# Kernel tuning notes

Measured on AMD Instinct MI355X. Metric: run time of the kernel, lower is better.

Reference implementation:

```python
import jax, jax.numpy as jnp
import numpy as np

# Dimensions (see shape_source): B=4, fine grid 8x8 windows of 16x16 tokens,
# pooled by 4x4 -> global grid 32x32 -> 2x2 windows of 16x16 tokens.
B, H, W, M, C, NH = 4, 8, 8, 16, 256, 8
HD = C // NH
GW = 2  # global window grid (2x2)


def _ln(x, g, b):
    m = x.mean(-1, keepdims=True)
    v = ((x - m) ** 2).mean(-1, keepdims=True)
    return (x - m) / jnp.sqrt(v + 1e-5) * g + b


def _posemb(x, w1, b1, w2):
    # RelativePositionEmbed: MLP(2 -> 512 -> C) over normalized 2D coords.
    N = x.shape[1]
    ctx = int(round(N ** 0.5))
    half = ctx // 2
    r = jnp.arange(ctx, dtype=x.dtype)
    grid = jnp.stack(jnp.meshgrid(r, r, indexing='ij'))  # [2, ctx, ctx]
    coords = ((grid - half) / half).reshape(2, -1).T     # [N, 2]
    return x + jax.nn.relu(coords @ w1 + b1) @ w2


def _mlp(x, w1, b1, w2, b2):
    return jax.nn.gelu(x @ w1 + b1, approximate=False) @ w2 + b2


def _sattn_block(x, ln1g, ln1b, wqkv, bqkv, wo, bo, ln2g, ln2b, mw1, mb1, mw2, mb2):
    # Pre-norm windowed MHSA + MLP (all2all self-attention inside each window).
    bn, N, _ = x.shape
    h = _ln(x, ln1g, ln1b)
    q, k, v = jnp.split(h @ wqkv + bqkv, 3, axis=-1)
    q = q.reshape(bn, N, NH, HD)
    k = k.reshape(bn, N, NH, HD)
    v = v.reshape(bn, N, NH, HD)
    att = jax.nn.softmax(jnp.einsum('bnhd,bmhd->bhnm', q, k) / (HD ** 0.5), axis=-1)
    o = jnp.einsum('bhnm,bmhd->bnhd', att, v).reshape(bn, N, C)
    x = x + o @ wo + bo
    return x + _mlp(_ln(x, ln2g, ln2b), mw1, mb1, mw2, mb2)


def _forward(scale0, scale1, pe_w1, pe_b1, pe_w2, ln1_g, ln1_b, wqkv, bqkv,
             wo, bo, ln2_g, ln2_b, mlp_w1, mlp_b1, mlp_w2, mlp_b2):
    # 1) per-scale relative position embeddings (weight_share=False path)
    x0 = _posemb(scale0, pe_w1[0], pe_b1[0], pe_w2[0])  # [B*64, 256, C]
    x1 = _posemb(scale1, pe_w1[1], pe_b1[1], pe_w2[1])  # [B*4, 256, C]

    # 2) propagate_bottom_up: max-pool each 16x16 window by 4 -> 4x4,
    p = x0.reshape(B * H * W, 4, 4, 4, 4, C).max(axis=(2, 4))  # (r1,p1,r2,p2)->max over p
    p = p.reshape(B, H, W, 4, 4, C).transpose(0, 1, 3, 2, 4, 5).reshape(B, H * 4, W * 4, C)
    l2g = p.reshape(B, GW, M, GW, M, C).transpose(0, 1, 3, 2, 4, 5).reshape(B * GW * GW, M * M, C)
    x1 = x1 + l2g

    # 3) all2all self-attention per scale (coarse to fine order; independent)
    o1 = _sattn_block(x1, ln1_g[1], ln1_b[1], wqkv[1], bqkv[1], wo[1], bo[1],
                      ln2_g[1], ln2_b[1], mlp_w1[1], mlp_b1[1], mlp_w2[1], mlp_b2[1])
    o0 = _sattn_block(x0, ln1_g[0], ln1_b[0], wqkv[0], bqkv[0], wo[0], bo[0],
                      ln2_g[0], ln2_b[0], mlp_w1[0], mlp_b1[0], mlp_w2[0], mlp_b2[0])

    # 4) one2one cross-attention aggregation: each global token queries the
    #    4x4 fine-token region it was pooled from (one-to-one mapping).
    fine = o0.reshape(B, H, W, 4, 4, 4, 4, C).transpose(0, 1, 2, 3, 5, 4, 6, 7)
    fine = fine.reshape(B * H * W * 16, 16, C)  # [B*1024, 16, C], order (b,h,w,r1,r2)
    g = o1.reshape(B, GW, GW, M, M, C).transpose(0, 1, 3, 2, 4, 5).reshape(B, 32, 32, C)
    g = g.reshape(B, H, 4, W, 4, C).transpose(0, 1, 3, 2, 4, 5).reshape(B * H * W * 16, 1, C)

    qn = _ln(g, ln1_g[1], ln1_b[1])
    kn = _ln(fine, ln1_g[1], ln1_b[1])
    wq, wk, wv = jnp.split(wqkv[1], 3, axis=-1)
    bq, bk, bv = jnp.split(bqkv[1], 3)
    q = (qn @ wq + bq).reshape(-1, 1, NH, HD)
    k = (kn @ wk + bk).reshape(-1, 16, NH, HD)
    v = (kn @ wv + bv).reshape(-1, 16, NH, HD)
    att = jax.nn.softmax(jnp.einsum('bnhd,bmhd->bhnm', q, k) / (HD ** 0.5), axis=-1)
    o = jnp.einsum('bhnm,bmhd->bnhd', att, v).reshape(-1, 1, C)
    g = g + o @ wo[1] + bo[1]
    g = g + _mlp(_ln(g, ln2_g[1], ln2_b[1]), mlp_w1[1], mlp_b1[1], mlp_w2[1], mlp_b2[1])

    # back to global window layout [B*4, 256, C]
    g = g.reshape(B, H, W, 4, 4, C).transpose(0, 1, 3, 2, 4, 5).reshape(B, 32, 32, C)
    o1 = g.reshape(B, GW, M, GW, M, C).transpose(0, 1, 3, 2, 4, 5).reshape(B * GW * GW, M * M, C)

    # concat on window axis so the harness sees a single output array
    return jnp.concatenate([o0, o1], axis=0)  # [272, 256, C]


def setup_inputs() -> dict:
    key = jax.random.key(0)
    ks = jax.random.split(key, 8)

    def w(k, shape):
        return jax.random.normal(k, shape, jnp.float32) * 0.02

    return {
        'scale0': jax.random.normal(ks[0], (B * H * W, M * M, C), jnp.float32),
        'scale1': jax.random.normal(ks[1], (B * GW * GW, M * M, C), jnp.float32),
        'pe_w1': w(ks[2], (2, 2, 512)), 'pe_b1': jnp.zeros((2, 512), jnp.float32),
        'pe_w2': w(ks[3], (2, 512, C)),
        'ln1_g': jnp.ones((2, C), jnp.float32), 'ln1_b': jnp.zeros((2, C), jnp.float32),
        'wqkv': w(ks[4], (2, C, 3 * C)), 'bqkv': jnp.zeros((2, 3 * C), jnp.float32),
        'wo': w(ks[5], (2, C, C)), 'bo': jnp.zeros((2, C), jnp.float32),
        'ln2_g': jnp.ones((2, C), jnp.float32), 'ln2_b': jnp.zeros((2, C), jnp.float32),
        'mlp_w1': w(ks[6], (2, C, 4 * C)), 'mlp_b1': jnp.zeros((2, 4 * C), jnp.float32),
        'mlp_w2': w(ks[7], (2, 4 * C, C)), 'mlp_b2': jnp.zeros((2, C), jnp.float32),
    }


def reference(scale0, scale1, pe_w1, pe_b1, pe_w2, ln1_g, ln1_b, wqkv, bqkv,
              wo, bo, ln2_g, ln2_b, mlp_w1, mlp_b1, mlp_w2, mlp_b2):
    return _forward(scale0, scale1, pe_w1, pe_b1, pe_w2, ln1_g, ln1_b, wqkv,
                    bqkv, wo, bo, ln2_g, ln2_b, mlp_w1, mlp_b1, mlp_w2, mlp_b2)
```

## Files before the change

### kernel.cpp

```cpp
#include <hip/hip_runtime.h>
#include <hip/hip_bf16.h>
#include <hip/hip_fp16.h>

#define ROWS0 65536
#define ROWS1 4096

typedef _Float16 half8 __attribute__((ext_vector_type(8)));
typedef _Float16 half4_t __attribute__((ext_vector_type(4)));
typedef float floatx4 __attribute__((ext_vector_type(4)));

#define LDSP(p) ((__attribute__((address_space(3))) void*)(p))
#define GLBP(p) ((const __attribute__((address_space(1))) void*)(p))

__device__ __forceinline__ float gelu_f(float x) {
    float t = x * (1.595769122f + 0.071354816f * x * x);
    return x / (1.0f + __expf(-t));
}

__global__ __launch_bounds__(256) void pe_kernel(
    const float* __restrict__ w1, const float* __restrict__ b1,
    const float* __restrict__ w2, float* __restrict__ pe)
{
    __shared__ float hid[512];
    int blk = blockIdx.x;
    int s = blk >> 8, n = blk & 255;
    int i = n >> 4, j = n & 15;
    float c0 = (i - 8) * 0.125f;
    float c1 = (j - 8) * 0.125f;
    int t = threadIdx.x;
    for (int hh = t; hh < 512; hh += 256) {
        float hv = c0 * w1[s * 1024 + hh] + c1 * w1[s * 1024 + 512 + hh] + b1[s * 512 + hh];
        hid[hh] = fmaxf(hv, 0.f);
    }
    __syncthreads();
    float o = 0.f;
    const float* w2p = w2 + (size_t)s * 512 * 256 + t;
    #pragma unroll 8
    for (int hh = 0; hh < 512; hh++) o += hid[hh] * w2p[hh * 256];
    pe[(size_t)s * 65536 + n * 256 + t] = o;
}

__global__ __launch_bounds__(256) void add_pe0_kernel(
    const float* __restrict__ s0, const float* __restrict__ pe, float* __restrict__ out)
{
    int row = blockIdx.x, c = threadIdx.x;
    out[(size_t)row * 256 + c] = s0[(size_t)row * 256 + c] + pe[(row & 255) * 256 + c];
}

__global__ __launch_bounds__(256) void pool_kernel(
    const float* __restrict__ x0, const float* __restrict__ s1,
    const float* __restrict__ pe1, float* __restrict__ x1out)
{
    int w1 = blockIdx.x >> 8, n1 = blockIdx.x & 255, c = threadIdx.x;
    int b = w1 >> 2, wy = (w1 >> 1) & 1, wx = w1 & 1;
    int ty = n1 >> 4, tx = n1 & 15;
    int gy = wy * 16 + ty, gx = wx * 16 + tx;
    int h = gy >> 2, r1 = gy & 3, w = gx >> 2, r2 = gx & 3;
    int fw = (b * 8 + h) * 8 + w;
    const float* base = x0 + ((size_t)fw * 256 + r1 * 64 + r2 * 4) * 256 + c;
    float mv = -1e30f;
    #pragma unroll
    for (int p1 = 0; p1 < 4; p1++)
        #pragma unroll
        for (int p2 = 0; p2 < 4; p2++)
            mv = fmaxf(mv, base[(p1 * 16 + p2) * 256]);
    size_t oidx = ((size_t)w1 * 256 + n1) * 256 + c;
    x1out[oidx] = s1[oidx] + pe1[n1 * 256 + c] + mv;
}

__global__ __launch_bounds__(256) void ln16_kernel(
    const float* __restrict__ X, const float* __restrict__ g,
    const float* __restrict__ b, _Float16* __restrict__ Y)
{
    __shared__ float smr[4];
    int row = blockIdx.x, t = threadIdx.x;
    float x = X[(size_t)row * 256 + t];
    float v = x;
    for (int o = 32; o; o >>= 1) v += __shfl_down(v, o);
    if ((t & 63) == 0) smr[t >> 6] = v;
    __syncthreads();
    float mean = (smr[0] + smr[1] + smr[2] + smr[3]) * (1.0f / 256.0f);
    __syncthreads();
    float d = x - mean;
    float vv = d * d;
    for (int o = 32; o; o >>= 1) vv += __shfl_down(vv, o);
    if ((t & 63) == 0) smr[t >> 6] = vv;
    __syncthreads();
    float var = (smr[0] + smr[1] + smr[2] + smr[3]) * (1.0f / 256.0f);
    float inv = 1.0f / sqrtf(var + 1e-5f);
    Y[(size_t)row * 256 + t] = (_Float16)(d * inv * g[t] + b[t]);
}

__global__ __launch_bounds__(256) void transposeW_kernel(
    const float* __restrict__ src, _Float16* __restrict__ dst, int K, int N)
{
    __shared__ float t[32][33];
    int k0 = blockIdx.y * 32, n0 = blockIdx.x * 32;
    int tx = threadIdx.x & 31, ty = threadIdx.x >> 5;
    for (int r = ty; r < 32; r += 8) t[r][tx] = src[(size_t)(k0 + r) * N + n0 + tx];
    __syncthreads();
    for (int r = ty; r < 32; r += 8) dst[(size_t)(n0 + r) * K + k0 + tx] = (_Float16)t[tx][r];
}

template<int ACT, int RES, int OUT16>
__global__ __launch_bounds__(256) void hgemm_kernel(
    const _Float16* __restrict__ A, const _Float16* __restrict__ Bw,
    const float* __restrict__ bias, const float* __restrict__ Res,
    void* __restrict__ Yv, int M, int N, int K)
{
    __shared__ alignas(16) _Float16 smem[4 * 4096];
    int tid = threadIdx.x;

    int gx = N >> 7;
    int nwg = gx * (M >> 7);
    int q8 = nwg >> 3;
    int wg = (blockIdx.x & 7) * q8 + (blockIdx.x >> 3);
    int m0 = (wg / gx) << 7, n0 = (wg % gx) << 7;

    int wave = tid >> 6, lane = tid & 63;
    int wr = wave >> 1, wc = wave & 1;
    int r = lane & 15, c = lane >> 4;
    floatx4 acc[4][4] = {};

    const int NT = K >> 5;

    auto stage = [&](int buf, int t) {
        int k0 = t << 5;
        #pragma unroll
        for (int p = 0; p < 2; p++) {
            int s = tid + (p << 8);
            int row = s >> 2, phys = s & 3;
            int logc = phys ^ (row & 3);
            const _Float16* ga = A + (size_t)(m0 + row) * K + k0 + logc * 8;
            __builtin_amdgcn_global_load_lds(GLBP(ga), LDSP(&smem[buf * 4096 + s * 8]), 16, 0, 0);
            const _Float16* gb = Bw + (size_t)(n0 + row) * K + k0 + logc * 8;
            __builtin_amdgcn_global_load_lds(GLBP(gb), LDSP(&smem[8192 + buf * 4096 + s * 8]), 16, 0, 0);
        }
    };

    stage(0, 0);
    __syncthreads();
    int cur = 0;
    for (int t = 0; t < NT; t++) {
        if (t + 1 < NT) stage(cur ^ 1, t + 1);
        const _Float16* As = &smem[cur * 4096];
        const _Float16* Bs = &smem[8192 + cur * 4096];
        half8 af[4], bf[4];
        #pragma unroll
        for (int i = 0; i < 4; i++) {
            int ra = wr * 64 + i * 16 + r;
            af[i] = *(const half8*)&As[ra * 32 + ((c ^ (ra & 3)) << 3)];
            int rb = wc * 64 + i * 16 + r;
            bf[i] = *(const half8*)&Bs[rb * 32 + ((c ^ (rb & 3)) << 3)];
        }
        #pragma unroll
        for (int i = 0; i < 4; i++)
            #pragma unroll
            for (int j = 0; j < 4; j++)
                acc[i][j] = __builtin_amdgcn_mfma_f32_16x16x32_f16(af[i], bf[j], acc[i][j], 0, 0, 0);
        __syncthreads();
        cur ^= 1;
    }

    int qrow = lane >> 4;
    if (OUT16) {
        _Float16* sth = smem + wave * 1152;
        #pragma unroll
        for (int i = 0; i < 4; i++) {
            #pragma unroll
            for (int j = 0; j < 4; j++) {
                float bj = bias[n0 + wc * 64 + j * 16 + r];
                #pragma unroll
                for (int reg = 0; reg < 4; reg++) {
                    float v = acc[i][j][reg] + bj;
                    if (ACT) v = gelu_f(v);
                    sth[(qrow * 4 + reg) * 72 + j * 16 + r] = (_Float16)v;
                }
            }
            #pragma unroll
            for (int p = 0; p < 2; p++) {
                int row = p * 8 + (lane >> 3);
                half8 hv = *(const half8*)&sth[row * 72 + (lane & 7) * 8];
                *(half8*)((_Float16*)Yv + (size_t)(m0 + wr * 64 + i * 16 + row) * N
                          + n0 + wc * 64 + (lane & 7) * 8) = hv;
            }
        }
    } else {
        float* stf = (float*)smem + wave * 1088;
        #pragma unroll
        for (int i = 0; i < 4; i++) {
            #pragma unroll
            for (int j = 0; j < 4; j++) {
                float bj = bias[n0 + wc * 64 + j * 16 + r];
                #pragma unroll
                for (int reg = 0; reg < 4; reg++) {
                    float v = acc[i][j][reg] + bj;
                    if (ACT) v = gelu_f(v);
                    stf[(qrow * 4 + reg) * 68 + j * 16 + r] = v;
                }
            }
            #pragma unroll
            for (int p = 0; p < 4; p++) {
                int row = p * 4 + (lane >> 4);
                float4 fv = *(const float4*)&stf[row * 68 + (lane & 15) * 4];
                size_t ga = (size_t)(m0 + wr * 64 + i * 16 + row) * N
                            + n0 + wc * 64 + (lane & 15) * 4;
                if (RES) {
                    float4 rv = *(const float4*)(Res + ga);
                    fv.x += rv.x; fv.y += rv.y; fv.z += rv.z; fv.w += rv.w;
                }
                *(float4*)((float*)Yv + ga) = fv;
            }
        }
    }
}

__global__ __launch_bounds__(256) void attn_mfma_kernel(
    const _Float16* __restrict__ qkv, _Float16* __restrict__ out)
{
    __shared__ alignas(16) _Float16 Klds[8192];
    __shared__ alignas(16) _Float16 Qlds[8192];
    __shared__ alignas(16) _Float16 VT[8192];
    __shared__ alignas(16) _Float16 Pl[4][4096];

    int tid = threadIdx.x;
    int win = blockIdx.x, head = blockIdx.y;
    int w = tid >> 6, lane = tid & 63;
    int r = lane & 15, h = lane >> 4;

    {
        const _Float16* base = qkv + ((size_t)(win * 256 + tid)) * 768 + head * 32;
        half8 qv[4], kv[4], vv[4];
        #pragma unroll
        for (int c = 0; c < 4; c++) {
            qv[c] = *(const half8*)(base + c * 8);
            kv[c] = *(const half8*)(base + 256 + c * 8);
            vv[c] = *(const half8*)(base + 512 + c * 8);
        }
        int rowbase = (tid >> 1) * 64;
        #pragma unroll
        for (int c = 0; c < 4; c++) {
            int phys = (((tid & 1) << 2) + c) ^ ((tid >> 1) & 7);
            *(half8*)&Qlds[rowbase + phys * 8] = qv[c];
            *(half8*)&Klds[rowbase + phys * 8] = kv[c];
        }
        #pragma unroll
        for (int d = 0; d < 32; d++)
            VT[d * 256 + (((tid >> 3) ^ (d & 7)) << 3) + (tid & 7)] = vv[d >> 3][d & 7];
    }
    __syncthreads();

    half8 vf[2][8];
    #pragma unroll
    for (int dc = 0; dc < 2; dc++)
        #pragma unroll
        for (int kc2 = 0; kc2 < 8; kc2++)
            vf[dc][kc2] = *(const half8*)&VT[(dc * 16 + r) * 256 + ((((kc2 << 2) + h) ^ (r & 7)) << 3)];

    const floatx4 zf = {0.f, 0.f, 0.f, 0.f};
    int physa = (((r & 1) << 2) + h) ^ ((r >> 1) & 7);

    for (int g = 0; g < 4; g++) {
        int qg = (w << 2) + g;
        half8 qb = *(const half8*)&Qlds[((qg << 3) + (r >> 1)) * 64 + physa * 8];
        floatx4 s[16];
        #pragma unroll
        for (int kc = 0; kc < 16; kc++) {
            half8 ka = *(const half8*)&Klds[((kc << 3) + (r >> 1)) * 64 + physa * 8];
            s[kc] = __builtin_amdgcn_mfma_f32_16x16x32_f16(ka, qb, zf, 0, 0, 0);
        }
        float m = -1e30f;
        #pragma unroll
        for (int kc = 0; kc < 16; kc++)
            #pragma unroll
            for (int e = 0; e < 4; e++) m = fmaxf(m, s[kc][e]);
        m = fmaxf(m, __shfl_xor(m, 16));
        m = fmaxf(m, __shfl_xor(m, 32));
        float l = 0.f;
        #pragma unroll
        for (int kc = 0; kc < 16; kc++)
            #pragma unroll
            for (int e = 0; e < 4; e++) {
                float p = __expf((s[kc][e] - m) * 0.17677669529663687f);
                s[kc][e] = p;
                l += p;
            }
        l += __shfl_xor(l, 16);
        l += __shfl_xor(l, 32);
        float inv = 1.0f / l;
        #pragma unroll
        for (int kc = 0; kc < 16; kc++) {
            half4_t pk;
            pk[0] = (_Float16)s[kc][0]; pk[1] = (_Float16)s[kc][1];
            pk[2] = (_Float16)s[kc][2]; pk[3] = (_Float16)s[kc][3];
            *(half4_t*)&Pl[w][r * 256 + ((((kc << 1) + (h >> 1)) ^ (r & 7)) << 3) + ((h & 1) << 2)] = pk;
        }
        floatx4 o0 = zf, o1 = zf;
        #pragma unroll
        for (int kc2 = 0; kc2 < 8; kc2++) {
            half8 pb = *(const half8*)&Pl[w][r * 256 + ((((kc2 << 2) + h) ^ (r & 7)) << 3)];
            o0 = __builtin_amdgcn_mfma_f32_16x16x32_f16(vf[0][kc2], pb, o0, 0, 0, 0);
            o1 = __builtin_amdgcn_mfma_f32_16x16x32_f16(vf[1][kc2], pb, o1, 0, 0, 0);
        }
        #pragma unroll
        for (int dc = 0; dc < 2; dc++) {
            floatx4 o = dc ? o1 : o0;
            half4_t oh;
            #pragma unroll
            for (int e = 0; e < 4; e++) oh[e] = (_Float16)(o[e] * inv);
            *(half4_t*)&Pl[w][(r >> 1) * 64 + (((((r & 1) << 2) + (dc << 1) + (h >> 1)) ^ ((r >> 1) & 7)) << 3) + ((h & 1) << 2)] = oh;
        }
        int q2 = lane >> 2, c2 = lane & 3;
        half8 ov = *(const half8*)&Pl[w][(q2 >> 1) * 64 + (((((q2 & 1) << 2) + c2) ^ ((q2 >> 1) & 7)) << 3)];
        *(half8*)(out + ((size_t)(win * 256 + qg * 16 + q2)) * 256 + head * 32 + c2 * 8) = ov;
    }
}

__global__ __launch_bounds__(128) void cross_attn_kernel(
    const _Float16* __restrict__ Qb, const _Float16* __restrict__ KV,
    _Float16* __restrict__ Ob, int fw0)
{
    __shared__ float att_s[8][16];
    int t = threadIdx.x;
    int lw = blockIdx.x >> 4;
    int sub = blockIdx.x & 15;
    int r1 = sub >> 2, r2 = sub & 3;
    int gi = (fw0 + lw) * 16 + sub;
    int h = t >> 4, m = t & 15;
    int p1 = m >> 2, p2 = m & 3;
    int lr = lw * 256 + r1 * 64 + p1 * 16 + r2 * 4 + p2;
    const half8* qp = (const half8*)(Qb + (size_t)gi * 256 + h * 32);
    const half8* kp = (const half8*)(KV + (size_t)lr * 512 + h * 32);
    float sc = 0.f;
    #pragma unroll
    for (int d8 = 0; d8 < 4; d8++) {
        half8 qv = qp[d8], kv = kp[d8];
        #pragma unroll
        for (int j = 0; j < 8; j++) sc += (float)qv[j] * (float)kv[j];
    }
    sc *= 0.17677669529663687f;
    float mx = sc;
    for (int o = 8; o; o >>= 1) mx = fmaxf(mx, __shfl_xor(mx, o));
    float e = __expf(sc - mx);
    float ssum = e;
    for (int o = 8; o; o >>= 1) ssum += __shfl_xor(ssum, o);
    att_s[h][m] = e / ssum;
    __syncthreads();
    int dg = t & 15;
    int d0 = dg * 2;
    float o0 = 0.f, o1 = 0.f;
    #pragma unroll
    for (int mm = 0; mm < 16; mm++) {
        int pp1 = mm >> 2, pp2 = mm & 3;
        int lrr = lw * 256 + r1 * 64 + pp1 * 16 + r2 * 4 + pp2;
        const _Float16* vp = KV + (size_t)lrr * 512 + 256 + h * 32;
        float a = att_s[h][mm];
        o0 += a * (float)vp[d0];
        o1 += a * (float)vp[d0 + 1];
    }
    Ob[(size_t)gi * 256 + h * 32 + d0]     = (_Float16)o0;
    Ob[(size_t)gi * 256 + h * 32 + d0 + 1] = (_Float16)o1;
}

__global__ __launch_bounds__(256) void gather_g_kernel(
    const float* __restrict__ o1, float* __restrict__ G)
{
    int gi = blockIdx.x, c = threadIdx.x;
    int b = gi >> 10, rem = gi & 1023;
    int h = rem >> 7, w = (rem >> 4) & 7, r1 = (rem >> 2) & 3, r2 = rem & 3;
    int gy = h * 4 + r1, gx = w * 4 + r2;
    int w1 = (b * 2 + (gy >> 4)) * 2 + (gx >> 4);
    int n1 = (gy & 15) * 16 + (gx & 15);
    G[(size_t)gi * 256 + c] = o1[((size_t)w1 * 256 + n1) * 256 + c];
}

__global__ __launch_bounds__(256) void scatter_g_kernel(
    const float* __restrict__ G, float* __restrict__ o1)
{
    int gi = blockIdx.x, c = threadIdx.x;
    int b = gi >> 10, rem = gi & 1023;
    int h = rem >> 7, w = (rem >> 4) & 7, r1 = (rem >> 2) & 3, r2 = rem & 3;
    int gy = h * 4 + r1, gx = w * 4 + r2;
    int w1 = (b * 2 + (gy >> 4)) * 2 + (gx >> 4);
    int n1 = (gy & 15) * 16 + (gx & 15);
    o1[((size_t)w1 * 256 + n1) * 256 + c] = G[(size_t)gi * 256 + c];
}

extern "C" void kernel_launch(void* const* d_in, const int* in_sizes, int n_in,
                              void* d_out, int out_size, void* d_ws, size_t ws_size,
                              hipStream_t stream)
{
    const float* scale0 = (const float*)d_in[0];
    const float* scale1 = (const float*)d_in[1];
    const float* pe_w1  = (const float*)d_in[2];
    const float* pe_b1  = (const float*)d_in[3];
    const float* pe_w2  = (const float*)d_in[4];
    const float* ln1_g  = (const float*)d_in[5];
    const float* ln1_b  = (const float*)d_in[6];
    const float* wqkv   = (const float*)d_in[7];
    const float* bqkv   = (const float*)d_in[8];
    const float* wo     = (const float*)d_in[9];
    const float* bo     = (const float*)d_in[10];
    const float* ln2_g  = (const float*)d_in[11];
    const float* ln2_b  = (const float*)d_in[12];
    const float* mw1    = (const float*)d_in[13];
    const float* mb1    = (const float*)d_in[14];
    const float* mw2    = (const float*)d_in[15];
    const float* mb2    = (const float*)d_in[16];
    float* out = (float*)d_out;
    char* arena = (char*)d_ws;

    float*    PE     = (float*)arena;              arena += 131072 * 4;
    float*    G      = (float*)arena;              arena += (size_t)4096 * 256 * 4;
    _Float16* Q16    = (_Float16*)arena;           arena += (size_t)4096 * 256 * 2;
    _Float16* OX16   = (_Float16*)arena;           arena += (size_t)4096 * 256 * 2;
    _Float16* wqkvT  = (_Float16*)arena;           arena += (size_t)2 * 768 * 256 * 2;
    _Float16* woT    = (_Float16*)arena;           arena += (size_t)2 * 256 * 256 * 2;
    _Float16* mw1T   = (_Float16*)arena;           arena += (size_t)2 * 1024 * 256 * 2;
    _Float16* mw2T   = (_Float16*)arena;           arena += (size_t)2 * 256 * 1024 * 2;
    size_t fixed_bytes = (size_t)(arena - (char*)d_ws);

    int R = 8192;
    if (fixed_bytes + (size_t)65536 * 4608 <= ws_size) R = 65536;
    else if (fixed_bytes + (size_t)32768 * 4608 <= ws_size) R = 32768;
    else if (fixed_bytes + (size_t)16384 * 4608 <= ws_size) R = 16384;
    int NC = 65536 / R;
    int CW = R / 256;

    _Float16* bufH16 = (_Float16*)arena;           arena += (size_t)R * 256 * 2;
    _Float16* qkv16  = (_Float16*)arena;           arena += (size_t)R * 768 * 2;
    _Float16* hid16  = (_Float16*)arena;           arena += (size_t)R * 1024 * 2;
    _Float16* o16    = (_Float16*)arena;

    auto hgemm = [&](const _Float16* A, const _Float16* Bw, const float* bias,
                     const float* Res, void* Y, int M, int N, int K, int act) {
        int nwg = (N >> 7) * (M >> 7);
        if (act)           hgemm_kernel<1, 0, 1><<<nwg, 256, 0, stream>>>(A, Bw, bias, nullptr, Y, M, N, K);
        else if (Res)      hgemm_kernel<0, 1, 0><<<nwg, 256, 0, stream>>>(A, Bw, bias, Res, Y, M, N, K);
        else               hgemm_kernel<0, 0, 1><<<nwg, 256, 0, stream>>>(A, Bw, bias, nullptr, Y, M, N, K);
    };

    auto sattn = [&](float* x, int Mrows, int nw, int s) {
        ln16_kernel<<<Mrows, 256, 0, stream>>>(x, ln1_g + s * 256, ln1_b + s * 256, bufH16);
        hgemm(bufH16, wqkvT + (size_t)s * 196608, bqkv + s * 768, nullptr, qkv16, Mrows, 768, 256, 0);
        attn_mfma_kernel<<<dim3(nw, 8), 256, 0, stream>>>(qkv16, o16);
        hgemm(o16, woT + (size_t)s * 65536, bo + s * 256, x, x, Mrows, 256, 256, 0);
        ln16_kernel<<<Mrows, 256, 0, stream>>>(x, ln2_g + s * 256, ln2_b + s * 256, bufH16);
        hgemm(bufH16, mw1T + (size_t)s * 262144, mb1 + s * 1024, nullptr, hid16, Mrows, 1024, 256, 1);
        hgemm(hid16, mw2T + (size_t)s * 262144, mb2 + s * 256, x, x, Mrows, 256, 1024, 0);
    };

    float* o1sec = out + (size_t)ROWS0 * 256;

    transposeW_kernel<<<dim3(768 / 32, 256 / 32), 256, 0, stream>>>(wqkv, wqkvT, 256, 768);
    transposeW_kernel<<<dim3(768 / 32, 256 / 32), 256, 0, stream>>>(wqkv + 196608, wqkvT + 196608, 256, 768);
    transposeW_kernel<<<dim3(256 / 32, 256 / 32), 256, 0, stream>>>(wo, woT, 256, 256);
    transposeW_kernel<<<dim3(256 / 32, 256 / 32), 256, 0, stream>>>(wo + 65536, woT + 65536, 256, 256);
    transposeW_kernel<<<dim3(1024 / 32, 256 / 32), 256, 0, stream>>>(mw1, mw1T, 256, 1024);
    transposeW_kernel<<<dim3(1024 / 32, 256 / 32), 256, 0, stream>>>(mw1 + 262144, mw1T + 262144, 256, 1024);
    transposeW_kernel<<<dim3(256 / 32, 1024 / 32), 256, 0, stream>>>(mw2, mw2T, 1024, 256);
    transposeW_kernel<<<dim3(256 / 32, 1024 / 32), 256, 0, stream>>>(mw2 + 262144, mw2T + 262144, 1024, 256);

    pe_kernel<<<512, 256, 0, stream>>>(pe_w1, pe_b1, pe_w2, PE);
    add_pe0_kernel<<<ROWS0, 256, 0, stream>>>(scale0, PE, out);
    pool_kernel<<<ROWS1, 256, 0, stream>>>(out, scale1, PE + 65536, o1sec);

    sattn(o1sec, ROWS1, 16, 1);
    for (int c = 0; c < NC; c++)
        sattn(out + (size_t)c * R * 256, R, CW, 0);

    gather_g_kernel<<<4096, 256, 0, stream>>>(o1sec, G);
    ln16_kernel<<<4096, 256, 0, stream>>>(G, ln1_g + 256, ln1_b + 256, bufH16);
    hgemm(bufH16, wqkvT + 196608, bqkv + 768, nullptr, Q16, 4096, 256, 256, 0);
    for (int c = 0; c < NC; c++) {
        float* xch = out + (size_t)c * R * 256;
        ln16_kernel<<<R, 256, 0, stream>>>(xch, ln1_g + 256, ln1_b + 256, bufH16);
        hgemm(bufH16, wqkvT + 196608 + 65536, bqkv + 768 + 256, nullptr, qkv16, R, 512, 256, 0);
        cross_attn_kernel<<<CW * 16, 128, 0, stream>>>(Q16, qkv16, OX16, c * CW);
    }
    hgemm(OX16, woT + 65536, bo + 256, G, G, 4096, 256, 256, 0);
    ln16_kernel<<<4096, 256, 0, stream>>>(G, ln2_g + 256, ln2_b + 256, bufH16);
    hgemm(bufH16, mw1T + 262144, mb1 + 1024, nullptr, hid16, 4096, 1024, 256, 1);
    hgemm(hid16, mw2T + 262144, mb2 + 256, G, G, 4096, 256, 1024, 0);
    scatter_g_kernel<<<4096, 256, 0, stream>>>(G, o1sec);
}
```

Baseline: 865.1 us.

## Use head-major QKV/output layout, split attention queries across two blocks, tree-reduce softmax

The QKV GEMM now writes its output in a head-major planar layout ([head][token][32]), and the attention kernel writes its output in that layout too. The output-projection GEMM reads its A operand in the same planar form, and cross-attention reads K/V from planes. Self-attention blocks now each handle half of a window's queries, which doubles the grid and halves Q shared memory. The P buffer is padded to reduce LDS bank conflicts, and the softmax max/sum reductions use a tree form with a fused scale. The aim is contiguous per-head loads, more parallelism and fewer LDS conflicts, at the cost of each block reloading K/V for its window.

```diff
diff --git a/kernel.cpp b/kernel.cpp
--- a/kernel.cpp
+++ b/kernel.cpp
@@ -16,6 +16,13 @@
     float t = x * (1.595769122f + 0.071354816f * x * x);
     return x / (1.0f + __expf(-t));
 }
+__device__ __forceinline__ floatx4 max4(floatx4 a, floatx4 b) {
+    floatx4 r;
+    r[0] = fmaxf(a[0], b[0]); r[1] = fmaxf(a[1], b[1]);
+    r[2] = fmaxf(a[2], b[2]); r[3] = fmaxf(a[3], b[3]);
+    return r;
+}
+__device__ __forceinline__ floatx4 add4(floatx4 a, floatx4 b) { return a + b; }
 
 __global__ __launch_bounds__(256) void pe_kernel(
     const float* __restrict__ w1, const float* __restrict__ b1,
@@ -102,11 +109,11 @@
     for (int r = ty; r < 32; r += 8) dst[(size_t)(n0 + r) * K + k0 + tx] = (_Float16)t[tx][r];
 }
 
-template<int ACT, int RES, int OUT16>
+template<int ACT, int RES, int OUT16, int ALAY, int OLAY>
 __global__ __launch_bounds__(256) void hgemm_kernel(
     const _Float16* __restrict__ A, const _Float16* __restrict__ Bw,
     const float* __restrict__ bias, const float* __restrict__ Res,
-    void* __restrict__ Yv, int M, int N, int K)
+    void* __restrict__ Yv, int M, int N, int K, size_t aps, size_t ops)
 {
     __shared__ alignas(16) _Float16 smem[4 * 4096];
     int tid = threadIdx.x;
@@ -131,7 +138,9 @@
             int s = tid + (p << 8);
             int row = s >> 2, phys = s & 3;
             int logc = phys ^ (row & 3);
-            const _Float16* ga = A + (size_t)(m0 + row) * K + k0 + logc * 8;
+            const _Float16* ga;
+            if (ALAY) ga = A + (size_t)(k0 >> 5) * aps + ((size_t)(m0 + row) << 5) + logc * 8;
+            else      ga = A + (size_t)(m0 + row) * K + k0 + logc * 8;
             __builtin_amdgcn_global_load_lds(GLBP(ga), LDSP(&smem[buf * 4096 + s * 8]), 16, 0, 0);
             const _Float16* gb = Bw + (size_t)(n0 + row) * K + k0 + logc * 8;
             __builtin_amdgcn_global_load_lds(GLBP(gb), LDSP(&smem[8192 + buf * 4096 + s * 8]), 16, 0, 0);
@@ -181,8 +190,12 @@
             for (int p = 0; p < 2; p++) {
                 int row = p * 8 + (lane >> 3);
                 half8 hv = *(const half8*)&sth[row * 72 + (lane & 7) * 8];
-                *(half8*)((_Float16*)Yv + (size_t)(m0 + wr * 64 + i * 16 + row) * N
-                          + n0 + wc * 64 + (lane & 7) * 8) = hv;
+                int grow = m0 + wr * 64 + i * 16 + row;
+                int col8 = n0 + wc * 64 + (lane & 7) * 8;
+                _Float16* dst;
+                if (OLAY) dst = (_Float16*)Yv + (size_t)(col8 >> 5) * ops + ((size_t)grow << 5) + (col8 & 31);
+                else      dst = (_Float16*)Yv + (size_t)grow * N + col8;
+                *(half8*)dst = hv;
             }
         }
     } else {
@@ -216,37 +229,40 @@
 }
 
 __global__ __launch_bounds__(256) void attn_mfma_kernel(
-    const _Float16* __restrict__ qkv, _Float16* __restrict__ out)
+    const _Float16* __restrict__ qkv, _Float16* __restrict__ out, const size_t ps)
 {
     __shared__ alignas(16) _Float16 Klds[8192];
-    __shared__ alignas(16) _Float16 Qlds[8192];
+    __shared__ alignas(16) _Float16 Qlds[4096];
     __shared__ alignas(16) _Float16 VT[8192];
-    __shared__ alignas(16) _Float16 Pl[4][4096];
+    __shared__ alignas(16) _Float16 Pl[4][4224];
 
     int tid = threadIdx.x;
-    int win = blockIdx.x, head = blockIdx.y;
+    int win = blockIdx.x >> 1, qhalf = blockIdx.x & 1, head = blockIdx.y;
     int w = tid >> 6, lane = tid & 63;
     int r = lane & 15, h = lane >> 4;
 
     {
-        const _Float16* base = qkv + ((size_t)(win * 256 + tid)) * 768 + head * 32;
-        half8 qv[4], kv[4], vv[4];
-        #pragma unroll
-        for (int c = 0; c < 4; c++) {
-            qv[c] = *(const half8*)(base + c * 8);
-            kv[c] = *(const half8*)(base + 256 + c * 8);
-            vv[c] = *(const half8*)(base + 512 + c * 8);
-        }
+        const half8* kp8 = (const half8*)(qkv + (size_t)(8 + head) * ps + (((size_t)win * 256 + tid) << 5));
+        const half8* vp8 = (const half8*)(qkv + (size_t)(16 + head) * ps + (((size_t)win * 256 + tid) << 5));
+        half8 kv[4], vv[4];
+        #pragma unroll
+        for (int c = 0; c < 4; c++) { kv[c] = kp8[c]; vv[c] = vp8[c]; }
         int rowbase = (tid >> 1) * 64;
         #pragma unroll
         for (int c = 0; c < 4; c++) {
             int phys = (((tid & 1) << 2) + c) ^ ((tid >> 1) & 7);
-            *(half8*)&Qlds[rowbase + phys * 8] = qv[c];
             *(half8*)&Klds[rowbase + phys * 8] = kv[c];
         }
         #pragma unroll
         for (int d = 0; d < 32; d++)
             VT[d * 256 + (((tid >> 3) ^ (d & 7)) << 3) + (tid & 7)] = vv[d >> 3][d & 7];
+        int local = tid >> 1;
+        const half8* qp8 = (const half8*)(qkv + (size_t)head * ps
+                            + (((size_t)win * 256 + qhalf * 128 + local) << 5) + (tid & 1) * 16);
+        half8 q0 = qp8[0], q1 = qp8[1];
+        int rb = (local >> 1) * 64, c0 = (tid & 1) * 2;
+        *(half8*)&Qlds[rb + (((((local & 1) << 2) + c0)) ^ ((local >> 1) & 7)) * 8] = q0;
+        *(half8*)&Qlds[rb + (((((local & 1) << 2) + c0 + 1)) ^ ((local >> 1) & 7)) * 8] = q1;
     }
     __syncthreads();
 
@@ -258,10 +274,11 @@
             vf[dc][kc2] = *(const half8*)&VT[(dc * 16 + r) * 256 + ((((kc2 << 2) + h) ^ (r & 7)) << 3)];
 
     const floatx4 zf = {0.f, 0.f, 0.f, 0.f};
+    const float SCALE = 0.17677669529663687f;
     int physa = (((r & 1) << 2) + h) ^ ((r >> 1) & 7);
 
-    for (int g = 0; g < 4; g++) {
-        int qg = (w << 2) + g;
+    for (int g = 0; g < 2; g++) {
+        int qg = (w << 1) + g;
         half8 qb = *(const half8*)&Qlds[((qg << 3) + (r >> 1)) * 64 + physa * 8];
         floatx4 s[16];
         #pragma unroll
@@ -269,22 +286,27 @@
             half8 ka = *(const half8*)&Klds[((kc << 3) + (r >> 1)) * 64 + physa * 8];
             s[kc] = __builtin_amdgcn_mfma_f32_16x16x32_f16(ka, qb, zf, 0, 0, 0);
         }
-        float m = -1e30f;
-        #pragma unroll
-        for (int kc = 0; kc < 16; kc++)
-            #pragma unroll
-            for (int e = 0; e < 4; e++) m = fmaxf(m, s[kc][e]);
+        floatx4 t8[8];
+        #pragma unroll
+        for (int i = 0; i < 8; i++) t8[i] = max4(s[2 * i], s[2 * i + 1]);
+        #pragma unroll
+        for (int i = 0; i < 4; i++) t8[i] = max4(t8[i], t8[i + 4]);
+        t8[0] = max4(max4(t8[0], t8[2]), max4(t8[1], t8[3]));
+        float m = fmaxf(fmaxf(t8[0][0], t8[0][1]), fmaxf(t8[0][2], t8[0][3]));
         m = fmaxf(m, __shfl_xor(m, 16));
         m = fmaxf(m, __shfl_xor(m, 32));
-        float l = 0.f;
+        float msc = m * SCALE;
         #pragma unroll
         for (int kc = 0; kc < 16; kc++)
             #pragma unroll
-            for (int e = 0; e < 4; e++) {
-                float p = __expf((s[kc][e] - m) * 0.17677669529663687f);
-                s[kc][e] = p;
-                l += p;
-            }
+            for (int e = 0; e < 4; e++)
+                s[kc][e] = __expf(fmaf(s[kc][e], SCALE, -msc));
+        #pragma unroll
+        for (int i = 0; i < 8; i++) t8[i] = add4(s[2 * i], s[2 * i + 1]);
+        #pragma unroll
+        for (int i = 0; i < 4; i++) t8[i] = add4(t8[i], t8[i + 4]);
+        t8[0] = add4(add4(t8[0], t8[2]), add4(t8[1], t8[3]));
+        float l = (t8[0][0] + t8[0][1]) + (t8[0][2] + t8[0][3]);
         l += __shfl_xor(l, 16);
         l += __shfl_xor(l, 32);
         float inv = 1.0f / l;
@@ -293,12 +315,12 @@
             half4_t pk;
             pk[0] = (_Float16)s[kc][0]; pk[1] = (_Float16)s[kc][1];
             pk[2] = (_Float16)s[kc][2]; pk[3] = (_Float16)s[kc][3];
-            *(half4_t*)&Pl[w][r * 256 + ((((kc << 1) + (h >> 1)) ^ (r & 7)) << 3) + ((h & 1) << 2)] = pk;
+            *(half4_t*)&Pl[w][r * 264 + ((((kc << 1) + (h >> 1)) ^ (r & 7)) << 3) + ((h & 1) << 2)] = pk;
         }
         floatx4 o0 = zf, o1 = zf;
         #pragma unroll
         for (int kc2 = 0; kc2 < 8; kc2++) {
-            half8 pb = *(const half8*)&Pl[w][r * 256 + ((((kc2 << 2) + h) ^ (r & 7)) << 3)];
+            half8 pb = *(const half8*)&Pl[w][r * 264 + ((((kc2 << 2) + h) ^ (r & 7)) << 3)];
             o0 = __builtin_amdgcn_mfma_f32_16x16x32_f16(vf[0][kc2], pb, o0, 0, 0, 0);
             o1 = __builtin_amdgcn_mfma_f32_16x16x32_f16(vf[1][kc2], pb, o1, 0, 0, 0);
         }
@@ -312,13 +334,14 @@
         }
         int q2 = lane >> 2, c2 = lane & 3;
         half8 ov = *(const half8*)&Pl[w][(q2 >> 1) * 64 + (((((q2 & 1) << 2) + c2) ^ ((q2 >> 1) & 7)) << 3)];
-        *(half8*)(out + ((size_t)(win * 256 + qg * 16 + q2)) * 256 + head * 32 + c2 * 8) = ov;
+        size_t tok = (size_t)win * 256 + qhalf * 128 + qg * 16 + q2;
+        *(half8*)(out + (size_t)head * ps + (tok << 5) + c2 * 8) = ov;
     }
 }
 
 __global__ __launch_bounds__(128) void cross_attn_kernel(
     const _Float16* __restrict__ Qb, const _Float16* __restrict__ KV,
-    _Float16* __restrict__ Ob, int fw0)
+    _Float16* __restrict__ Ob, int fw0, const size_t ps)
 {
     __shared__ float att_s[8][16];
     int t = threadIdx.x;
@@ -330,7 +353,7 @@
     int p1 = m >> 2, p2 = m & 3;
     int lr = lw * 256 + r1 * 64 + p1 * 16 + r2 * 4 + p2;
     const half8* qp = (const half8*)(Qb + (size_t)gi * 256 + h * 32);
-    const half8* kp = (const half8*)(KV + (size_t)lr * 512 + h * 32);
+    const half8* kp = (const half8*)(KV + (size_t)h * ps + ((size_t)lr << 5));
     float sc = 0.f;
     #pragma unroll
     for (int d8 = 0; d8 < 4; d8++) {
@@ -353,7 +376,7 @@
     for (int mm = 0; mm < 16; mm++) {
         int pp1 = mm >> 2, pp2 = mm & 3;
         int lrr = lw * 256 + r1 * 64 + pp1 * 16 + r2 * 4 + pp2;
-        const _Float16* vp = KV + (size_t)lrr * 512 + 256 + h * 32;
+        const _Float16* vp = KV + (size_t)(8 + h) * ps + ((size_t)lrr << 5);
         float a = att_s[h][mm];
         o0 += a * (float)vp[d0];
         o1 += a * (float)vp[d0 + 1];
@@ -433,21 +456,30 @@
     _Float16* o16    = (_Float16*)arena;
 
     auto hgemm = [&](const _Float16* A, const _Float16* Bw, const float* bias,
-                     const float* Res, void* Y, int M, int N, int K, int act) {
+                     const float* Res, void* Y, int M, int N, int K, int act,
+                     int alay, int olay, size_t aps, size_t ops) {
         int nwg = (N >> 7) * (M >> 7);
-        if (act)           hgemm_kernel<1, 0, 1><<<nwg, 256, 0, stream>>>(A, Bw, bias, nullptr, Y, M, N, K);
-        else if (Res)      hgemm_kernel<0, 1, 0><<<nwg, 256, 0, stream>>>(A, Bw, bias, Res, Y, M, N, K);
-        else               hgemm_kernel<0, 0, 1><<<nwg, 256, 0, stream>>>(A, Bw, bias, nullptr, Y, M, N, K);
+        if (act)
+            hgemm_kernel<1, 0, 1, 0, 0><<<nwg, 256, 0, stream>>>(A, Bw, bias, nullptr, Y, M, N, K, 0, 0);
+        else if (Res && alay)
+            hgemm_kernel<0, 1, 0, 1, 0><<<nwg, 256, 0, stream>>>(A, Bw, bias, Res, Y, M, N, K, aps, 0);
+        else if (Res)
+            hgemm_kernel<0, 1, 0, 0, 0><<<nwg, 256, 0, stream>>>(A, Bw, bias, Res, Y, M, N, K, 0, 0);
+        else if (olay)
+            hgemm_kernel<0, 0, 1, 0, 1><<<nwg, 256, 0, stream>>>(A, Bw, bias, nullptr, Y, M, N, K, 0, ops);
+        else
+            hgemm_kernel<0, 0, 1, 0, 0><<<nwg, 256, 0, stream>>>(A, Bw, bias, nullptr, Y, M, N, K, 0, 0);
     };
 
     auto sattn = [&](float* x, int Mrows, int nw, int s) {
+        size_t ps = (size_t)Mrows * 32;
         ln16_kernel<<<Mrows, 256, 0, stream>>>(x, ln1_g + s * 256, ln1_b + s * 256, bufH16);
-        hgemm(bufH16, wqkvT + (size_t)s * 196608, bqkv + s * 768, nullptr, qkv16, Mrows, 768, 256, 0);
-        attn_mfma_kernel<<<dim3(nw, 8), 256, 0, stream>>>(qkv16, o16);
-        hgemm(o16, woT + (size_t)s * 65536, bo + s * 256, x, x, Mrows, 256, 256, 0);
+        hgemm(bufH16, wqkvT + (size_t)s * 196608, bqkv + s * 768, nullptr, qkv16, Mrows, 768, 256, 0, 0, 1, 0, ps);
+        attn_mfma_kernel<<<dim3(nw * 2, 8), 256, 0, stream>>>(qkv16, o16, ps);
+        hgemm(o16, woT + (size_t)s * 65536, bo + s * 256, x, x, Mrows, 256, 256, 0, 1, 0, ps, 0);
         ln16_kernel<<<Mrows, 256, 0, stream>>>(x, ln2_g + s * 256, ln2_b + s * 256, bufH16);
-        hgemm(bufH16, mw1T + (size_t)s * 262144, mb1 + s * 1024, nullptr, hid16, Mrows, 1024, 256, 1);
-        hgemm(hid16, mw2T + (size_t)s * 262144, mb2 + s * 256, x, x, Mrows, 256, 1024, 0);
+        hgemm(bufH16, mw1T + (size_t)s * 262144, mb1 + s * 1024, nullptr, hid16, Mrows, 1024, 256, 1, 0, 0, 0, 0);
+        hgemm(hid16, mw2T + (size_t)s * 262144, mb2 + s * 256, x, x, Mrows, 256, 1024, 0, 0, 0, 0, 0);
     };
 
     float* o1sec = out + (size_t)ROWS0 * 256;
@@ -471,16 +503,17 @@
 
     gather_g_kernel<<<4096, 256, 0, stream>>>(o1sec, G);
     ln16_kernel<<<4096, 256, 0, stream>>>(G, ln1_g + 256, ln1_b + 256, bufH16);
-    hgemm(bufH16, wqkvT + 196608, bqkv + 768, nullptr, Q16, 4096, 256, 256, 0);
+    hgemm(bufH16, wqkvT + 196608, bqkv + 768, nullptr, Q16, 4096, 256, 256, 0, 0, 0, 0, 0);
     for (int c = 0; c < NC; c++) {
         float* xch = out + (size_t)c * R * 256;
+        size_t ps = (size_t)R * 32;
         ln16_kernel<<<R, 256, 0, stream>>>(xch, ln1_g + 256, ln1_b + 256, bufH16);
-        hgemm(bufH16, wqkvT + 196608 + 65536, bqkv + 768 + 256, nullptr, qkv16, R, 512, 256, 0);
-        cross_attn_kernel<<<CW * 16, 128, 0, stream>>>(Q16, qkv16, OX16, c * CW);
-    }
-    hgemm(OX16, woT + 65536, bo + 256, G, G, 4096, 256, 256, 0);
+        hgemm(bufH16, wqkvT + 196608 + 65536, bqkv + 768 + 256, nullptr, qkv16, R, 512, 256, 0, 0, 1, 0, ps);
+        cross_attn_kernel<<<CW * 16, 128, 0, stream>>>(Q16, qkv16, OX16, c * CW, ps);
+    }
+    hgemm(OX16, woT + 65536, bo + 256, G, G, 4096, 256, 256, 0, 0, 0, 0, 0);
     ln16_kernel<<<4096, 256, 0, stream>>>(G, ln2_g + 256, ln2_b + 256, bufH16);
-    hgemm(bufH16, mw1T + 262144, mb1 + 1024, nullptr, hid16, 4096, 1024, 256, 1);
-    hgemm(hid16, mw2T + 262144, mb2 + 256, G, G, 4096, 256, 1024, 0);
+    hgemm(bufH16, mw1T + 262144, mb1 + 1024, nullptr, hid16, 4096, 1024, 256, 1, 0, 0, 0, 0);
+    hgemm(hid16, mw2T + 262144, mb2 + 256, G, G, 4096, 256, 1024, 0, 0, 0, 0, 0);
     scatter_g_kernel<<<4096, 256, 0, stream>>>(G, o1sec);
 }
```

Measured after the change: 893.1 us. 3.2% more time.
